# Kernel tuning notes

Measured on AMD Instinct MI355X. Metric: run time of the kernel, lower is better.

The kernel has to match this reference:

```python
import jax, jax.numpy as jnp
import numpy as np

N = 4_194_304
L = 15
SLOPE = 0.01  # torch LeakyReLU default


def setup_inputs() -> dict:
    key = jax.random.key(0)
    ks = jax.random.split(key, 16)
    n = jax.random.normal
    return {
        "x": n(ks[0], (N, 2), jnp.float32),
        # scale Linear(1,1) per layer (small init keeps exp(log_scale) stable)
        "scale_w": n(ks[1], (L, 1, 1), jnp.float32) * 0.2,
        "scale_b": n(ks[2], (L, 1), jnp.float32) * 0.1,
        # g_theta_scale: 1->32->16->1
        "sW1": n(ks[3], (L, 1, 32), jnp.float32) * 0.5,
        "sb1": n(ks[4], (L, 32), jnp.float32) * 0.1,
        "sW2": n(ks[5], (L, 32, 16), jnp.float32) * 0.2,
        "sb2": n(ks[6], (L, 16), jnp.float32) * 0.1,
        "sW3": n(ks[7], (L, 16, 1), jnp.float32) * 0.2,
        "sb3": n(ks[8], (L, 1), jnp.float32) * 0.1,
        # g_theta_shift: 1->32->16->1
        "tW1": n(ks[9], (L, 1, 32), jnp.float32) * 0.5,
        "tb1": n(ks[10], (L, 32), jnp.float32) * 0.1,
        "tW2": n(ks[11], (L, 32, 16), jnp.float32) * 0.2,
        "tb2": n(ks[12], (L, 16), jnp.float32) * 0.1,
        "tW3": n(ks[13], (L, 16, 1), jnp.float32) * 0.2,
        "tb3": n(ks[14], (L, 1), jnp.float32) * 0.1,
    }


def _mlp(h, W1, b1, W2, b2, W3, b3):
    h = jax.nn.leaky_relu(h @ W1 + b1, SLOPE)
    h = jax.nn.leaky_relu(h @ W2 + b2, SLOPE)
    return h @ W3 + b3


def reference(x, scale_w, scale_b, sW1, sb1, sW2, sb2, sW3, sb3,
              tW1, tb1, tW2, tb2, tW3, tb3):
    def step(carry, p):
        z1, z2, ld = carry
        sw, sb, w1, b1, w2, b2, w3, b3, u1, c1, u2, c2, u3, c3 = p
        x1, x2 = z2, z1  # swap
        log_scale = jnp.tanh(_mlp(x1, w1, b1, w2, b2, w3, b3)) @ sw + sb
        z2n = jnp.exp(log_scale) * x2 + _mlp(x1, u1, c1, u2, c2, u3, c3)
        return (x1, z2n, ld + log_scale), None

    init = (x[:, 1:2], x[:, 0:1], jnp.zeros_like(x[:, :1]))
    params = (scale_w, scale_b, sW1, sb1, sW2, sb2, sW3, sb3,
              tW1, tb1, tW2, tb2, tW3, tb3)
    (z1, z2, ld), _ = jax.lax.scan(step, init, params)
    return jnp.concatenate((z1, z2), axis=1), ld
```

## Files before the change

kernel.cpp:

```cpp
#include <hip/hip_runtime.h>
#include <math.h>

#define SLOPE 0.01f
#define NLAYER 15
#define FINE_CELLS 512
#define COARSE_CELLS 128
#define CELLS 640
#define FINE_NODES 513
#define NODES_PER_NET 642
#define TABLE_FLOAT4 (NLAYER * CELLS)

__device__ __forceinline__ float mlp_exact(
    float x1,
    const float* __restrict__ W1, const float* __restrict__ b1,
    const float* __restrict__ W2, const float* __restrict__ b2,
    const float* __restrict__ W3, float b3)
{
    float h2[16];
#pragma unroll
    for (int n = 0; n < 16; ++n) h2[n] = b2[n];
#pragma unroll 2
    for (int j = 0; j < 32; ++j) {
        float h = fmaf(W1[j], x1, b1[j]);
        h = fmaxf(h, SLOPE * h);
#pragma unroll
        for (int n = 0; n < 16; ++n) h2[n] = fmaf(h, W2[j * 16 + n], h2[n]);
    }
    float o = b3;
#pragma unroll
    for (int n = 0; n < 16; ++n) {
        float h = fmaxf(h2[n], SLOPE * h2[n]);
        o = fmaf(h, W3[n], o);
    }
    return o;
}

__global__ __launch_bounds__(640) void build_tables(
    const float* __restrict__ scale_w, const float* __restrict__ scale_b,
    const float* __restrict__ sW1, const float* __restrict__ sb1,
    const float* __restrict__ sW2, const float* __restrict__ sb2,
    const float* __restrict__ sW3, const float* __restrict__ sb3,
    const float* __restrict__ tW1, const float* __restrict__ tb1,
    const float* __restrict__ tW2, const float* __restrict__ tb2,
    const float* __restrict__ tW3, const float* __restrict__ tb3,
    float* __restrict__ ws)
{
    const int m = blockIdx.x;
    const int l = m >> 1;
    const int which = m & 1;
    const float* W1 = (which ? tW1 : sW1) + l * 32;
    const float* b1 = (which ? tb1 : sb1) + l * 32;
    const float* W2 = (which ? tW2 : sW2) + l * 512;
    const float* b2 = (which ? tb2 : sb2) + l * 16;
    const float* W3 = (which ? tW3 : sW3) + l * 16;
    const float  b3 = which ? tb3[l] : sb3[l];

    __shared__ float nodes[NODES_PER_NET];

    for (int i = threadIdx.x; i < NODES_PER_NET; i += blockDim.x) {
        const float x = (i < FINE_NODES) ? (-2.0f + (float)i * (1.0f / 128.0f))
                                         : (-32.0f + (float)(i - FINE_NODES) * 0.5f);
        float o = mlp_exact(x, W1, b1, W2, b2, W3, b3);
        nodes[i] = which ? o : fmaf(tanhf(o), scale_w[l], scale_b[l]);
    }
    __syncthreads();

    for (int c = threadIdx.x; c < CELLS; c += blockDim.x) {
        const int base = (c < FINE_CELLS) ? c : (FINE_NODES + (c - FINE_CELLS));
        float2 v = make_float2(nodes[base], nodes[base + 1]);
        *(float2*)(ws + ((size_t)(l * CELLS + c) * 4) + which * 2) = v;
    }
}

__device__ __forceinline__ void layer_eval(const float4* __restrict__ T, float x1,
                                           float* ls, float* g)
{
    float uf = fmaf(x1, 128.0f, 256.0f);
    float uc = fmaf(x1, 2.0f, 576.0f);
    bool fine = (fabsf(x1) < 2.0f);
    float fu = fine ? floorf(uf)
                    : fminf(fmaxf(floorf(uc), 512.0f), 639.0f);
    float u  = fine ? uf : uc;
    float t  = u - fu;
    float4 c = T[(int)fu];
    *ls = fmaf(c.y - c.x, t, c.x);
    *g  = fmaf(c.w - c.z, t, c.z);
}

__global__ __launch_bounds__(1024) void flow_lut(
    const float4* __restrict__ x,
    const float4* __restrict__ ws,
    float4* __restrict__ out_z,
    float2* __restrict__ out_ld,
    int npair)
{
    __shared__ float4 lds[TABLE_FLOAT4];
    for (int i = threadIdx.x; i < TABLE_FLOAT4; i += blockDim.x) lds[i] = ws[i];
    __syncthreads();

    const int stride = gridDim.x * blockDim.x;
    for (int p = blockIdx.x * blockDim.x + threadIdx.x; p < npair; p += stride) {
        float4 xi = x[p];
        float az1 = xi.y, az2 = xi.x, ald = 0.0f;
        float bz1 = xi.w, bz2 = xi.z, bld = 0.0f;
#pragma unroll
        for (int l = 0; l < NLAYER; ++l) {
            const float4* T = lds + l * CELLS;
            float ax1 = az2, ax2 = az1;
            float bx1 = bz2, bx2 = bz1;
            float als, ag, bls, bg;
            layer_eval(T, ax1, &als, &ag);
            layer_eval(T, bx1, &bls, &bg);
            az1 = ax1; az2 = fmaf(__expf(als), ax2, ag); ald += als;
            bz1 = bx1; bz2 = fmaf(__expf(bls), bx2, bg); bld += bls;
        }
        out_z[p]  = make_float4(az1, az2, bz1, bz2);
        out_ld[p] = make_float2(ald, bld);
    }
}

extern "C" void kernel_launch(void* const* d_in, const int* in_sizes, int n_in,
                              void* d_out, int out_size, void* d_ws, size_t ws_size,
                              hipStream_t stream) {
    const int n = in_sizes[0] / 2;
    const int npair = n / 2;

    const float4* x       = (const float4*)d_in[0];
    const float*  scale_w = (const float*)d_in[1];
    const float*  scale_b = (const float*)d_in[2];
    const float*  sW1     = (const float*)d_in[3];
    const float*  sb1     = (const float*)d_in[4];
    const float*  sW2     = (const float*)d_in[5];
    const float*  sb2     = (const float*)d_in[6];
    const float*  sW3     = (const float*)d_in[7];
    const float*  sb3     = (const float*)d_in[8];
    const float*  tW1     = (const float*)d_in[9];
    const float*  tb1     = (const float*)d_in[10];
    const float*  tW2     = (const float*)d_in[11];
    const float*  tb2     = (const float*)d_in[12];
    const float*  tW3     = (const float*)d_in[13];
    const float*  tb3     = (const float*)d_in[14];

    float4* out_z  = (float4*)d_out;
    float2* out_ld = (float2*)((float*)d_out + (size_t)2 * n);

    build_tables<<<30, 640, 0, stream>>>(scale_w, scale_b,
        sW1, sb1, sW2, sb2, sW3, sb3,
        tW1, tb1, tW2, tb2, tW3, tb3, (float*)d_ws);

    flow_lut<<<256, 1024, 0, stream>>>(x, (const float4*)d_ws, out_z, out_ld, npair);
}
```

Measured before the change: 151.0 us.

## Store LUT as shared nodes to halve LDS and use exp2 with doubled grid

The lookup table now stores per-node float2 values instead of per-cell float4 pairs. This roughly halves shared memory per block, so more blocks can be resident per CU, and the grid is doubled to use that. Log-scale values are prescaled by 1/ln2 so the hardware exp2 can be used directly, with the log-det rescaled once at output. Each lookup now needs two LDS reads instead of one.

```diff
diff --git a/kernel.cpp b/kernel.cpp
--- a/kernel.cpp
+++ b/kernel.cpp
@@ -3,12 +3,19 @@
 
 #define SLOPE 0.01f
 #define NLAYER 15
-#define FINE_CELLS 512
-#define COARSE_CELLS 128
-#define CELLS 640
 #define FINE_NODES 513
 #define NODES_PER_NET 642
-#define TABLE_FLOAT4 (NLAYER * CELLS)
+#define TABLE_F2 (NLAYER * NODES_PER_NET)
+#define INV_LN2 1.4426950408889634f
+#define LN2F 0.6931471805599453f
+
+__device__ __forceinline__ float fast_exp2(float x) {
+#if __has_builtin(__builtin_amdgcn_exp2f)
+    return __builtin_amdgcn_exp2f(x);
+#else
+    return __expf(x * LN2F);
+#endif
+}
 
 __device__ __forceinline__ float mlp_exact(
     float x1,
@@ -55,47 +62,44 @@
     const float* W3 = (which ? tW3 : sW3) + l * 16;
     const float  b3 = which ? tb3[l] : sb3[l];
 
-    __shared__ float nodes[NODES_PER_NET];
-
     for (int i = threadIdx.x; i < NODES_PER_NET; i += blockDim.x) {
         const float x = (i < FINE_NODES) ? (-2.0f + (float)i * (1.0f / 128.0f))
                                          : (-32.0f + (float)(i - FINE_NODES) * 0.5f);
         float o = mlp_exact(x, W1, b1, W2, b2, W3, b3);
-        nodes[i] = which ? o : fmaf(tanhf(o), scale_w[l], scale_b[l]);
-    }
-    __syncthreads();
-
-    for (int c = threadIdx.x; c < CELLS; c += blockDim.x) {
-        const int base = (c < FINE_CELLS) ? c : (FINE_NODES + (c - FINE_CELLS));
-        float2 v = make_float2(nodes[base], nodes[base + 1]);
-        *(float2*)(ws + ((size_t)(l * CELLS + c) * 4) + which * 2) = v;
+        float v = which ? o : fmaf(tanhf(o), scale_w[l], scale_b[l]) * INV_LN2;
+        ws[(size_t)((l * NODES_PER_NET + i) * 2 + which)] = v;
     }
 }
 
-__device__ __forceinline__ void layer_eval(const float4* __restrict__ T, float x1,
-                                           float* ls, float* g)
+__device__ __forceinline__ void layer_eval(const float2* __restrict__ Nl, float x1,
+                                           float* ls2, float* g)
 {
     float uf = fmaf(x1, 128.0f, 256.0f);
-    float uc = fmaf(x1, 2.0f, 576.0f);
+    float uc = fmaf(x1, 2.0f, 577.0f);
     bool fine = (fabsf(x1) < 2.0f);
-    float fu = fine ? floorf(uf)
-                    : fminf(fmaxf(floorf(uc), 512.0f), 639.0f);
+    float bf = fine ? floorf(uf)
+                    : fminf(fmaxf(floorf(uc), 513.0f), 640.0f);
     float u  = fine ? uf : uc;
-    float t  = u - fu;
-    float4 c = T[(int)fu];
-    *ls = fmaf(c.y - c.x, t, c.x);
-    *g  = fmaf(c.w - c.z, t, c.z);
+    float t  = u - bf;
+    int i = (int)bf;
+    float2 lo = Nl[i];
+    float2 hi = Nl[i + 1];
+    *ls2 = fmaf(hi.x - lo.x, t, lo.x);
+    *g   = fmaf(hi.y - lo.y, t, lo.y);
 }
 
-__global__ __launch_bounds__(1024) void flow_lut(
+__global__ __launch_bounds__(1024, 8) void flow_lut(
     const float4* __restrict__ x,
     const float4* __restrict__ ws,
     float4* __restrict__ out_z,
     float2* __restrict__ out_ld,
     int npair)
 {
-    __shared__ float4 lds[TABLE_FLOAT4];
-    for (int i = threadIdx.x; i < TABLE_FLOAT4; i += blockDim.x) lds[i] = ws[i];
+    __shared__ __align__(16) float2 NT[TABLE_F2];
+    {
+        float4* dst = (float4*)NT;
+        for (int i = threadIdx.x; i < TABLE_F2 / 2; i += blockDim.x) dst[i] = ws[i];
+    }
     __syncthreads();
 
     const int stride = gridDim.x * blockDim.x;
@@ -105,17 +109,17 @@
         float bz1 = xi.w, bz2 = xi.z, bld = 0.0f;
 #pragma unroll
         for (int l = 0; l < NLAYER; ++l) {
-            const float4* T = lds + l * CELLS;
-            float ax1 = az2, ax2 = az1;
-            float bx1 = bz2, bx2 = bz1;
+            const float2* Nl = NT + l * NODES_PER_NET;
             float als, ag, bls, bg;
-            layer_eval(T, ax1, &als, &ag);
-            layer_eval(T, bx1, &bls, &bg);
-            az1 = ax1; az2 = fmaf(__expf(als), ax2, ag); ald += als;
-            bz1 = bx1; bz2 = fmaf(__expf(bls), bx2, bg); bld += bls;
+            layer_eval(Nl, az2, &als, &ag);
+            layer_eval(Nl, bz2, &bls, &bg);
+            float az2n = fmaf(fast_exp2(als), az1, ag);
+            float bz2n = fmaf(fast_exp2(bls), bz1, bg);
+            az1 = az2; az2 = az2n; ald += als;
+            bz1 = bz2; bz2 = bz2n; bld += bls;
         }
         out_z[p]  = make_float4(az1, az2, bz1, bz2);
-        out_ld[p] = make_float2(ald, bld);
+        out_ld[p] = make_float2(ald * LN2F, bld * LN2F);
     }
 }
 
@@ -148,5 +152,5 @@
         sW1, sb1, sW2, sb2, sW3, sb3,
         tW1, tb1, tW2, tb2, tW3, tb3, (float*)d_ws);
 
-    flow_lut<<<256, 1024, 0, stream>>>(x, (const float4*)d_ws, out_z, out_ld, npair);
+    flow_lut<<<512, 1024, 0, stream>>>(x, (const float4*)d_ws, out_z, out_ld, npair);
 }
```

Result: slower. 160.4 us (+6.2%).

## Stream per-layer LUT through double-buffered LDS and store slope/intercept tables

Applied to the files above, without the earlier changes.

Instead of copying the full 15-layer table into shared memory before any work, each block keeps two layer-sized buffers and loads the next layer's table while it evaluates the current one. Each thread now handles 4 pairs in registers. Tables store slope/intercept pairs so interpolation is one FMA, and log-scales are pre-multiplied by 1/ln2 so exp2 can be used. The aim is to cut the large upfront LDS fill, raise occupancy with a smaller LDS footprint, and shorten the per-element math, at the cost of a barrier per layer and many more blocks, each reloading every table.

```diff
diff --git a/kernel.cpp b/kernel.cpp
--- a/kernel.cpp
+++ b/kernel.cpp
@@ -8,7 +8,18 @@
 #define CELLS 640
 #define FINE_NODES 513
 #define NODES_PER_NET 642
-#define TABLE_FLOAT4 (NLAYER * CELLS)
+#define INV_LN2 1.4426950408889634f
+#define LN2F 0.6931471805599453f
+#define TPB 512
+#define PAIRS 4
+
+__device__ __forceinline__ float fast_exp2(float x) {
+#if __has_builtin(__builtin_amdgcn_exp2f)
+    return __builtin_amdgcn_exp2f(x);
+#else
+    return __expf(x * LN2F);
+#endif
+}
 
 __device__ __forceinline__ float mlp_exact(
     float x1,
@@ -61,61 +72,87 @@
         const float x = (i < FINE_NODES) ? (-2.0f + (float)i * (1.0f / 128.0f))
                                          : (-32.0f + (float)(i - FINE_NODES) * 0.5f);
         float o = mlp_exact(x, W1, b1, W2, b2, W3, b3);
-        nodes[i] = which ? o : fmaf(tanhf(o), scale_w[l], scale_b[l]);
+        nodes[i] = which ? o : fmaf(tanhf(o), scale_w[l], scale_b[l]) * INV_LN2;
     }
     __syncthreads();
 
     for (int c = threadIdx.x; c < CELLS; c += blockDim.x) {
-        const int base = (c < FINE_CELLS) ? c : (FINE_NODES + (c - FINE_CELLS));
-        float2 v = make_float2(nodes[base], nodes[base + 1]);
-        *(float2*)(ws + ((size_t)(l * CELLS + c) * 4) + which * 2) = v;
+        int base; float x_lo, invh;
+        if (c < FINE_CELLS) { base = c;     x_lo = -2.0f  + (float)c * (1.0f / 128.0f); invh = 128.0f; }
+        else                { base = c + 1; x_lo = -32.0f + (float)(c - FINE_CELLS) * 0.5f; invh = 2.0f; }
+        float lo = nodes[base], hi = nodes[base + 1];
+        float slope = (hi - lo) * invh;
+        float icpt  = fmaf(-slope, x_lo, lo);
+        *(float2*)(ws + ((size_t)(l * CELLS + c) * 4) + which * 2) = make_float2(slope, icpt);
     }
 }
 
-__device__ __forceinline__ void layer_eval(const float4* __restrict__ T, float x1,
-                                           float* ls, float* g)
-{
-    float uf = fmaf(x1, 128.0f, 256.0f);
-    float uc = fmaf(x1, 2.0f, 576.0f);
-    bool fine = (fabsf(x1) < 2.0f);
+__device__ __forceinline__ int cell_index(float x) {
+    float uf = fmaf(x, 128.0f, 256.0f);
+    float uc = fmaf(x, 2.0f, 576.0f);
+    bool fine = (fabsf(x) < 2.0f);
     float fu = fine ? floorf(uf)
                     : fminf(fmaxf(floorf(uc), 512.0f), 639.0f);
-    float u  = fine ? uf : uc;
-    float t  = u - fu;
-    float4 c = T[(int)fu];
-    *ls = fmaf(c.y - c.x, t, c.x);
-    *g  = fmaf(c.w - c.z, t, c.z);
+    return (int)fu;
 }
 
-__global__ __launch_bounds__(1024) void flow_lut(
+__device__ __forceinline__ void couple(const float4* __restrict__ T,
+                                       float& z1, float& z2, float& ld)
+{
+    float4 c = T[cell_index(z2)];
+    float ls = fmaf(c.x, z2, c.y);
+    float g  = fmaf(c.z, z2, c.w);
+    float z2n = fmaf(fast_exp2(ls), z1, g);
+    z1 = z2; z2 = z2n; ld += ls;
+}
+
+__global__ __launch_bounds__(TPB, 8) void flow_lut(
     const float4* __restrict__ x,
     const float4* __restrict__ ws,
     float4* __restrict__ out_z,
     float2* __restrict__ out_ld,
     int npair)
 {
-    __shared__ float4 lds[TABLE_FLOAT4];
-    for (int i = threadIdx.x; i < TABLE_FLOAT4; i += blockDim.x) lds[i] = ws[i];
+    __shared__ __align__(16) float4 buf[2][CELLS];
+    const int nthreads = gridDim.x * blockDim.x;
+    const int tid0 = blockIdx.x * blockDim.x + threadIdx.x;
+
+    for (int i = threadIdx.x; i < CELLS; i += TPB) buf[0][i] = ws[i];
+
+    float az1[PAIRS], az2[PAIRS], ald[PAIRS];
+    float bz1[PAIRS], bz2[PAIRS], bld[PAIRS];
+#pragma unroll
+    for (int k = 0; k < PAIRS; ++k) {
+        int p = tid0 + k * nthreads;
+        float4 xi = (p < npair) ? x[p] : make_float4(0.f, 0.f, 0.f, 0.f);
+        az1[k] = xi.y; az2[k] = xi.x; ald[k] = 0.f;
+        bz1[k] = xi.w; bz2[k] = xi.z; bld[k] = 0.f;
+    }
     __syncthreads();
 
-    const int stride = gridDim.x * blockDim.x;
-    for (int p = blockIdx.x * blockDim.x + threadIdx.x; p < npair; p += stride) {
-        float4 xi = x[p];
-        float az1 = xi.y, az2 = xi.x, ald = 0.0f;
-        float bz1 = xi.w, bz2 = xi.z, bld = 0.0f;
 #pragma unroll
-        for (int l = 0; l < NLAYER; ++l) {
-            const float4* T = lds + l * CELLS;
-            float ax1 = az2, ax2 = az1;
-            float bx1 = bz2, bx2 = bz1;
-            float als, ag, bls, bg;
-            layer_eval(T, ax1, &als, &ag);
-            layer_eval(T, bx1, &bls, &bg);
-            az1 = ax1; az2 = fmaf(__expf(als), ax2, ag); ald += als;
-            bz1 = bx1; bz2 = fmaf(__expf(bls), bx2, bg); bld += bls;
+    for (int l = 0; l < NLAYER; ++l) {
+        if (l + 1 < NLAYER) {
+            const float4* src = ws + (size_t)(l + 1) * CELLS;
+            for (int i = threadIdx.x; i < CELLS; i += TPB)
+                buf[(l + 1) & 1][i] = src[i];
         }
-        out_z[p]  = make_float4(az1, az2, bz1, bz2);
-        out_ld[p] = make_float2(ald, bld);
+        const float4* T = buf[l & 1];
+#pragma unroll
+        for (int k = 0; k < PAIRS; ++k) {
+            couple(T, az1[k], az2[k], ald[k]);
+            couple(T, bz1[k], bz2[k], bld[k]);
+        }
+        __syncthreads();
+    }
+
+#pragma unroll
+    for (int k = 0; k < PAIRS; ++k) {
+        int p = tid0 + k * nthreads;
+        if (p < npair) {
+            out_z[p]  = make_float4(az1[k], az2[k], bz1[k], bz2[k]);
+            out_ld[p] = make_float2(ald[k] * LN2F, bld[k] * LN2F);
+        }
     }
 }
 
@@ -148,5 +185,6 @@
         sW1, sb1, sW2, sb2, sW3, sb3,
         tW1, tb1, tW2, tb2, tW3, tb3, (float*)d_ws);
 
-    flow_lut<<<256, 1024, 0, stream>>>(x, (const float4*)d_ws, out_z, out_ld, npair);
+    const int nblocks = (npair + TPB * PAIRS - 1) / (TPB * PAIRS);
+    flow_lut<<<nblocks, TPB, 0, stream>>>(x, (const float4*)d_ws, out_z, out_ld, npair);
 }
```

After: 537.3 us. 256% more time.
